# Optimization experiments

Hardware: AMD Instinct MI355X
Metric: run time of the kernel (lower is better)

The kernel has to match this reference:

```python
import jax, jax.numpy as jnp
import numpy as np
from jax import lax

B, S, F, D, H, L, A = 16, 512, 64, 512, 8, 4, 3
E = D // H  # head_dim = 64

def _gelu(t):
    return jax.nn.gelu(t, approximate=False)  # torch nn.GELU() is exact erf

def _make_masks():
    i = jnp.arange(S)[:, None]
    j = jnp.arange(S)[None, :]
    d = jnp.abs(i - j)
    ms = []
    for h in range(min(5, H)):
        dil = 2 ** h
        ms.append((d <= dil) | (d % (2 ** (h + 1)) == 0))
    m = jnp.stack(ms)  # [5,S,S] bool
    idx = jnp.minimum(jnp.arange(H), m.shape[0] - 1)
    return m[idx]  # [H,S,S]

MASKS = _make_masks()

def _ln(x, g, b, eps=1e-5):
    mu = jnp.mean(x, -1, keepdims=True)
    var = jnp.mean((x - mu) ** 2, -1, keepdims=True)
    return (x - mu) * lax.rsqrt(var + eps) * g + b

def _conv1d(x_ncw, w, b):
    y = lax.conv_general_dilated(x_ncw, w, (1,), [(1, 1)],
                                 dimension_numbers=("NCH", "OIH", "NCH"))
    return y + b[None, :, None]

def _attn(x, Wq, bq, Wk, bk, Wv, bv, Wo, bo):
    # x: [B,S,D]; Wq/Wk/Wv: [H,E,D] (stacked per-head Linear weights)
    q = jnp.einsum("bsd,hed->bhse", x, Wq) + bq[None, :, None, :]
    k = jnp.einsum("bsd,hed->bhse", x, Wk) + bk[None, :, None, :]
    v = jnp.einsum("bsd,hed->bhse", x, Wv) + bv[None, :, None, :]
    s = jnp.einsum("bhse,bhte->bhst", q, k) / (E ** 0.5)
    s = jnp.where(MASKS[None], s, -jnp.inf)  # log-sparse masked_fill
    p = jax.nn.softmax(s, axis=-1)
    o = jnp.einsum("bhst,bhte->bhse", p, v)
    o = o.transpose(0, 2, 1, 3).reshape(x.shape[0], x.shape[1], D)  # concat heads
    return o @ Wo.T + bo

def _forward(x, conv1_w, conv1_b, conv2_w, conv2_b, emb_w, emb_b, pos,
             Wq, bq, Wk, bk, Wv, bv, Wo, bo, ln1_g, ln1_b, ln2_g, ln2_b,
             W1, b1, W2, b2, lnf_g, lnf_b,
             a1_w, a1_b, a2_w, a2_b, a3_w, a3_b, a4_w, a4_b,
             c1_w, c1_b, c2_w, c2_b, c3_w, c3_b, c4_w, c4_b):
    # feature extractor: two conv1d+GELU over time axis
    h0 = _gelu(_conv1d(x.transpose(0, 2, 1), conv1_w, conv1_b))
    h0 = _gelu(_conv1d(h0, conv2_w, conv2_b)).transpose(0, 2, 1)  # [B,S,D]
    z = h0 @ emb_w.T + emb_b + pos[:, :S]  # input embedding + positional
    for l in range(L):  # PyraFormer blocks (pre-norm residual)
        z = z + _attn(_ln(z, ln1_g[l], ln1_b[l]),
                      Wq[l], bq[l], Wk[l], bk[l], Wv[l], bv[l], Wo[l], bo[l])
        h = _ln(z, ln2_g[l], ln2_b[l])
        z = z + (_gelu(h @ W1[l].T + b1[l]) @ W2[l].T + b2[l])
    z = _ln(z, lnf_g, lnf_b)
    feat = z[:, -1, :]  # last timestep features

    def head(f, layers):
        (w1, bb1), (w2, bb2), (w3, bb3), (w4, bb4) = layers
        f = _gelu(f @ w1.T + bb1)
        f = _gelu(f @ w2.T + bb2)
        f = _gelu(f @ w3.T + bb3)
        return f @ w4.T + bb4

    policy = head(feat, [(a1_w, a1_b), (a2_w, a2_b), (a3_w, a3_b), (a4_w, a4_b)])
    value = head(feat, [(c1_w, c1_b), (c2_w, c2_b), (c3_w, c3_b), (c4_w, c4_b)])
    return policy, value

def setup_inputs() -> dict:
    key = jax.random.key(0)
    ks = iter(jax.random.split(key, 64))
    r = lambda shape, s=0.05: jax.random.normal(next(ks), shape, jnp.float32) * s
    return {
        "x": jax.random.normal(next(ks), (B, S, F), jnp.float32),
        "conv1_w": r((D // 2, F, 3)), "conv1_b": jnp.zeros((D // 2,)),
        "conv2_w": r((D, D // 2, 3)), "conv2_b": jnp.zeros((D,)),
        "emb_w": r((D, D)), "emb_b": jnp.zeros((D,)),
        "pos": r((1, S, D), 0.02),
        "Wq": r((L, H, E, D)), "bq": jnp.zeros((L, H, E)),
        "Wk": r((L, H, E, D)), "bk": jnp.zeros((L, H, E)),
        "Wv": r((L, H, E, D)), "bv": jnp.zeros((L, H, E)),
        "Wo": r((L, D, D)), "bo": jnp.zeros((L, D)),
        "ln1_g": jnp.ones((L, D)), "ln1_b": jnp.zeros((L, D)),
        "ln2_g": jnp.ones((L, D)), "ln2_b": jnp.zeros((L, D)),
        "W1": r((L, 4 * D, D)), "b1": jnp.zeros((L, 4 * D)),
        "W2": r((L, D, 4 * D)), "b2": jnp.zeros((L, D)),
        "lnf_g": jnp.ones((D,)), "lnf_b": jnp.zeros((D,)),
        "a1_w": r((128, D)), "a1_b": jnp.zeros((128,)),
        "a2_w": r((256, 128)), "a2_b": jnp.zeros((256,)),
        "a3_w": r((57, 256)), "a3_b": jnp.zeros((57,)),
        "a4_w": r((A, 57)), "a4_b": jnp.zeros((A,)),
        "c1_w": r((128, D)), "c1_b": jnp.zeros((128,)),
        "c2_w": r((256, 128)), "c2_b": jnp.zeros((256,)),
        "c3_w": r((57, 256)), "c3_b": jnp.zeros((57,)),
        "c4_w": r((1, 57)), "c4_b": jnp.zeros((1,)),
    }

def reference(x, conv1_w, conv1_b, conv2_w, conv2_b, emb_w, emb_b, pos,
              Wq, bq, Wk, bk, Wv, bv, Wo, bo, ln1_g, ln1_b, ln2_g, ln2_b,
              W1, b1, W2, b2, lnf_g, lnf_b,
              a1_w, a1_b, a2_w, a2_b, a3_w, a3_b, a4_w, a4_b,
              c1_w, c1_b, c2_w, c2_b, c3_w, c3_b, c4_w, c4_b):
    return _forward(x, conv1_w, conv1_b, conv2_w, conv2_b, emb_w, emb_b, pos,
                    Wq, bq, Wk, bk, Wv, bv, Wo, bo, ln1_g, ln1_b, ln2_g, ln2_b,
                    W1, b1, W2, b2, lnf_g, lnf_b,
                    a1_w, a1_b, a2_w, a2_b, a3_w, a3_b, a4_w, a4_b,
                    c1_w, c1_b, c2_w, c2_b, c3_w, c3_b, c4_w, c4_b)
```

## Files before the change

kernel.cpp:

```cpp
#include <hip/hip_runtime.h>
#include <hip/hip_bf16.h>
#include <cstdint>

typedef __attribute__((ext_vector_type(8))) short bf16x8;
typedef __attribute__((ext_vector_type(4))) float f32x4;
typedef unsigned short u16;

#define DEV __device__ __forceinline__

DEV float b2f(u16 u) {
  union { unsigned int i; float f; } v; v.i = ((unsigned int)u) << 16; return v.f;
}
DEV u16 f2b(float f) {
  __hip_bfloat16 h = __float2bfloat16(f);
  return *reinterpret_cast<u16*>(&h);
}
DEV float erf_fast(float x) {
  float ax = fabsf(x);
  float t = __builtin_amdgcn_rcpf(fmaf(0.3275911f, ax, 1.0f));
  float p = t * fmaf(t, fmaf(t, fmaf(t, fmaf(t, 1.061405429f, -1.453152027f),
                                     1.421413741f), -0.284496736f), 0.254829592f);
  float r = fmaf(-p, __expf(-ax * ax), 1.0f);
  return copysignf(r, x);
}
DEV float gelu_f(float x) { return 0.5f * x * (1.0f + erf_fast(x * 0.70710678118654752f)); }

DEV void async_cp16(const u16* g, u16* l) {
  __builtin_amdgcn_global_load_lds(
      (const __attribute__((address_space(1))) void*)g,
      (__attribute__((address_space(3))) void*)l, 16, 0, 0);
}

__global__ void probe_kernel(const unsigned int* __restrict__ g, int* __restrict__ flag) {
  if (threadIdx.x == 0 && blockIdx.x == 0) *flag = (*g == 0x3F800000u) ? 1 : 0;
}

struct CvtArgs {
  const void* src[42];
  unsigned int off[43];
};

struct alignas(16) U8v { u16 u[8]; };
struct alignas(8)  U4v { u16 u[4]; };

__global__ __launch_bounds__(256) void cvt_kernel(CvtArgs a, int n_t, unsigned int total,
                                                  const int* __restrict__ flag,
                                                  u16* __restrict__ dst) {
  unsigned int i8 = (blockIdx.x * 256u + threadIdx.x) * 8u;
  if (i8 >= total) return;
  int t = 0;
  while (t + 1 < n_t && i8 >= a.off[t + 1]) t++;
  unsigned int j = i8 - a.off[t];
  bool in_seg = (i8 + 8 <= a.off[t + 1]) && (i8 + 8 <= total);
  int fp32 = *flag;
  if (fp32) {
    if (in_seg && ((j & 3) == 0)) {
      const float* s = (const float*)a.src[t] + j;
      float4 v0 = *(const float4*)s;
      float4 v1 = *(const float4*)(s + 4);
      U8v o;
      o.u[0] = f2b(v0.x); o.u[1] = f2b(v0.y); o.u[2] = f2b(v0.z); o.u[3] = f2b(v0.w);
      o.u[4] = f2b(v1.x); o.u[5] = f2b(v1.y); o.u[6] = f2b(v1.z); o.u[7] = f2b(v1.w);
      *(U8v*)(dst + i8) = o;
    } else {
      for (int k = 0; k < 8; k++) {
        unsigned int i = i8 + k;
        if (i >= total) break;
        int tt = t;
        while (tt + 1 < n_t && i >= a.off[tt + 1]) tt++;
        dst[i] = f2b(((const float*)a.src[tt])[i - a.off[tt]]);
      }
    }
  } else {
    if (in_seg && ((j & 7) == 0)) {
      *(U8v*)(dst + i8) = *(const U8v*)((const u16*)a.src[t] + j);
    } else {
      for (int k = 0; k < 8; k++) {
        unsigned int i = i8 + k;
        if (i >= total) break;
        int tt = t;
        while (tt + 1 < n_t && i >= a.off[tt + 1]) tt++;
        dst[i] = ((const u16*)a.src[tt])[i - a.off[tt]];
      }
    }
  }
}

__global__ __launch_bounds__(256) void gemm_bt44(
    const u16* __restrict__ A, const u16* __restrict__ W,
    const u16* __restrict__ bias,
    u16* __restrict__ outB, float* __restrict__ outF,
    int N, int K, int mode)
{
  __shared__ __align__(16) u16 As[2][64 * 32];
  __shared__ __align__(16) u16 Bs[2][64 * 32];
  int t = threadIdx.x, l = t & 63, w = t >> 6;
  int wr = w >> 1, wc = w & 1;
  int col = l & 15, quad = l >> 4;
  int q8 = (quad ^ ((col >> 1) & 3)) * 8;
  int m0 = blockIdx.x * 64;
  int n0 = blockIdx.y * 64;

  f32x4 acc[2][2];
#pragma unroll
  for (int i = 0; i < 2; i++)
#pragma unroll
    for (int j = 0; j < 2; j++) acc[i][j] = (f32x4){0.f, 0.f, 0.f, 0.f};

  int ra = t >> 2;
  int ca = (t & 3) ^ ((ra >> 1) & 3);
  const u16* a1 = A + (size_t)(m0 + ra) * K + ca * 8;
  const u16* b1 = W + (size_t)(n0 + ra) * K + ca * 8;

  int nK = K >> 5;
  async_cp16(a1, &As[0][t * 8]);
  async_cp16(b1, &Bs[0][t * 8]);
  for (int ki = 0; ki < nK; ki++) {
    int cur = ki & 1;
    if (ki + 1 < nK) {
      int nxt = cur ^ 1, kt = (ki + 1) << 5;
      async_cp16(a1 + kt, &As[nxt][t * 8]);
      async_cp16(b1 + kt, &Bs[nxt][t * 8]);
      __builtin_amdgcn_s_waitcnt(0x0F72);
    } else {
      __builtin_amdgcn_s_waitcnt(0x0F70);
    }
    __builtin_amdgcn_s_barrier();
    __builtin_amdgcn_sched_barrier(0);
    bf16x8 af[2], bfv[2];
#pragma unroll
    for (int mi = 0; mi < 2; mi++)
      af[mi] = *(const bf16x8*)&As[cur][(wr * 32 + mi * 16 + col) * 32 + q8];
#pragma unroll
    for (int ni = 0; ni < 2; ni++)
      bfv[ni] = *(const bf16x8*)&Bs[cur][(wc * 32 + ni * 16 + col) * 32 + q8];
#pragma unroll
    for (int mi = 0; mi < 2; mi++)
#pragma unroll
      for (int ni = 0; ni < 2; ni++)
        acc[mi][ni] = __builtin_amdgcn_mfma_f32_16x16x32_bf16(bfv[ni], af[mi], acc[mi][ni], 0, 0, 0);
    __builtin_amdgcn_sched_barrier(0);
    __builtin_amdgcn_s_barrier();
  }

  int mBase = m0 + wr * 32, nBase = n0 + wc * 32;
  if (mode == 1) {
#pragma unroll
    for (int mi = 0; mi < 2; mi++) {
      int m = mBase + mi * 16 + col;
      size_t rowOff = (size_t)m * N;
#pragma unroll
      for (int ni = 0; ni < 2; ni++) {
        int n4 = nBase + ni * 16 + quad * 4;
        U4v bb = *(const U4v*)&bias[n4];
        f32x4 v = acc[mi][ni];
        U4v o;
#pragma unroll
        for (int r = 0; r < 4; r++) o.u[r] = f2b(gelu_f(v[r] + b2f(bb.u[r])));
        *(U4v*)&outB[rowOff + n4] = o;
      }
    }
  } else {
#pragma unroll
    for (int mi = 0; mi < 2; mi++) {
      int m = mBase + mi * 16 + col;
      size_t rowOff = (size_t)m * N;
#pragma unroll
      for (int ni = 0; ni < 2; ni++) {
        int n4 = nBase + ni * 16 + quad * 4;
        U4v bb = *(const U4v*)&bias[n4];
        f32x4 v = acc[mi][ni];
        float4* p = (float4*)&outF[rowOff + n4];
        float4 zv = *p;
        zv.x += v[0] + b2f(bb.u[0]);
        zv.y += v[1] + b2f(bb.u[1]);
        zv.z += v[2] + b2f(bb.u[2]);
        zv.w += v[3] + b2f(bb.u[3]);
        *p = zv;
      }
    }
  }
}

__global__ __launch_bounds__(256) void gemm_qkv64(
    const u16* __restrict__ A,
    const u16* __restrict__ Wq, const u16* __restrict__ Wk, const u16* __restrict__ Wv,
    const u16* __restrict__ bq, const u16* __restrict__ bk, const u16* __restrict__ bv,
    u16* __restrict__ outQ, u16* __restrict__ outK, u16* __restrict__ outVT, int K)
{
  __shared__ __align__(16) u16 As[2][64 * 32];
  __shared__ __align__(16) u16 Bs[2][128 * 32];
  int t = threadIdx.x, l = t & 63, w = t >> 6;
  int wr = w >> 1, wc = w & 1;
  int col = l & 15, quad = l >> 4;
  int q8 = (quad ^ ((col >> 1) & 3)) * 8;
  int m0 = blockIdx.x * 64;
  int sel = blockIdx.y >> 2;
  int n0 = (blockIdx.y & 3) * 128;
  const u16* W = sel == 0 ? Wq : (sel == 1 ? Wk : Wv);
  const u16* bias = sel == 0 ? bq : (sel == 1 ? bk : bv);
  const bool swp = (sel < 2);
  const float scl = sel == 0 ? 0.125f : 1.0f;

  f32x4 acc[2][4];
#pragma unroll
  for (int i = 0; i < 2; i++)
#pragma unroll
    for (int j = 0; j < 4; j++) acc[i][j] = (f32x4){0.f, 0.f, 0.f, 0.f};

  int ra = t >> 2;
  int ca = (t & 3) ^ ((ra >> 1) & 3);
  int g1i = t, g2i = t + 256;
  int rb1 = g1i >> 2, rb2 = g2i >> 2;
  int cb1 = (g1i & 3) ^ ((rb1 >> 1) & 3);
  int cb2 = (g2i & 3) ^ ((rb2 >> 1) & 3);
  const u16* a1 = A + (size_t)(m0 + ra) * K + ca * 8;
  const u16* b1 = W + (size_t)(n0 + rb1) * K + cb1 * 8;
  const u16* b2 = W + (size_t)(n0 + rb2) * K + cb2 * 8;

  int nK = K >> 5;
  async_cp16(a1, &As[0][t * 8]);
  async_cp16(b1, &Bs[0][g1i * 8]);
  async_cp16(b2, &Bs[0][g2i * 8]);
  for (int ki = 0; ki < nK; ki++) {
    int cur = ki & 1;
    if (ki + 1 < nK) {
      int nxt = cur ^ 1, kt = (ki + 1) << 5;
      async_cp16(a1 + kt, &As[nxt][t * 8]);
      async_cp16(b1 + kt, &Bs[nxt][g1i * 8]);
      async_cp16(b2 + kt, &Bs[nxt][g2i * 8]);
      __builtin_amdgcn_s_waitcnt(0x0F73);
    } else {
      __builtin_amdgcn_s_waitcnt(0x0F70);
    }
    __builtin_amdgcn_s_barrier();
    __builtin_amdgcn_sched_barrier(0);
    bf16x8 af[2], bfv[4];
#pragma unroll
    for (int mi = 0; mi < 2; mi++)
      af[mi] = *(const bf16x8*)&As[cur][(wr * 32 + mi * 16 + col) * 32 + q8];
#pragma unroll
    for (int ni = 0; ni < 4; ni++)
      bfv[ni] = *(const bf16x8*)&Bs[cur][(wc * 64 + ni * 16 + col) * 32 + q8];
    if (swp) {
#pragma unroll
      for (int mi = 0; mi < 2; mi++)
#pragma unroll
        for (int ni = 0; ni < 4; ni++)
          acc[mi][ni] = __builtin_amdgcn_mfma_f32_16x16x32_bf16(bfv[ni], af[mi], acc[mi][ni], 0, 0, 0);
    } else {
#pragma unroll
      for (int mi = 0; mi < 2; mi++)
#pragma unroll
        for (int ni = 0; ni < 4; ni++)
          acc[mi][ni] = __builtin_amdgcn_mfma_f32_16x16x32_bf16(af[mi], bfv[ni], acc[mi][ni], 0, 0, 0);
    }
    __builtin_amdgcn_sched_barrier(0);
    __builtin_amdgcn_s_barrier();
  }

  int mBase = m0 + wr * 32, nBase = n0 + wc * 64;
  if (swp) {
    u16* outB = sel == 0 ? outQ : outK;
#pragma unroll
    for (int mi = 0; mi < 2; mi++) {
      int m = mBase + mi * 16 + col;
      size_t rowOff = (size_t)m * 512;
#pragma unroll
      for (int ni = 0; ni < 4; ni++) {
        int n4 = nBase + ni * 16 + quad * 4;
        U4v bb = *(const U4v*)&bias[n4];
        f32x4 v = acc[mi][ni];
        U4v o;
#pragma unroll
        for (int r = 0; r < 4; r++) o.u[r] = f2b((v[r] + b2f(bb.u[r])) * scl);
        *(U4v*)&outB[rowOff + n4] = o;
      }
    }
  } else {
    int b = m0 >> 9;
    int sB = m0 & 511;
#pragma unroll
    for (int mi = 0; mi < 2; mi++) {
      int s4 = sB + wr * 32 + mi * 16 + quad * 4;
#pragma unroll
      for (int ni = 0; ni < 4; ni++) {
        int n = nBase + ni * 16 + col;
        int h = n >> 6, e = n & 63;
        float bvv = b2f(bias[n]);
        f32x4 v = acc[mi][ni];
        U4v o;
#pragma unroll
        for (int r = 0; r < 4; r++) o.u[r] = f2b(v[r] + bvv);
        *(U4v*)&outVT[((size_t)((b * 8 + h) * 64 + e)) * 512 + s4] = o;
      }
    }
  }
}

__global__ __launch_bounds__(256) void zinit_kernel(const u16* __restrict__ pos,
                                                    float* __restrict__ z)
{
  int i = (blockIdx.x * 256 + threadIdx.x) * 8;
  int n = i & 511;
  int m = i >> 9;
  int s = m & 511;
  U8v p = *(const U8v*)&pos[s * 512 + n];
  float4 o0 = {b2f(p.u[0]), b2f(p.u[1]), b2f(p.u[2]), b2f(p.u[3])};
  float4 o1 = {b2f(p.u[4]), b2f(p.u[5]), b2f(p.u[6]), b2f(p.u[7])};
  *(float4*)(z + i) = o0;
  *(float4*)(z + i + 4) = o1;
}

__global__ void im2col3_kernel(const u16* __restrict__ src,
                               u16* __restrict__ dst, int C)
{
  int m = blockIdx.x;
  int k = blockIdx.y * blockDim.x + threadIdx.x;
  int ci = k / 3;
  int tap = k - ci * 3;
  int s = m & 511;
  int sp = s + tap - 1;
  u16 val = 0;
  if (sp >= 0 && sp < 512) val = src[(size_t)(m + tap - 1) * C + ci];
  dst[(size_t)m * (3 * C) + k] = val;
}

__global__ __launch_bounds__(256) void ln_kernel(
    const float* __restrict__ z, const u16* __restrict__ gam,
    const u16* __restrict__ bet, u16* __restrict__ out)
{
  int w = threadIdx.x >> 6, l = threadIdx.x & 63;
  int row = blockIdx.x * 4 + w;
  const float* zr = z + (size_t)row * 512;
  float4 v0 = *(const float4*)(zr + l * 8);
  float4 v1 = *(const float4*)(zr + l * 8 + 4);
  float x[8] = {v0.x, v0.y, v0.z, v0.w, v1.x, v1.y, v1.z, v1.w};
  float s = 0.f;
#pragma unroll
  for (int i = 0; i < 8; i++) s += x[i];
#pragma unroll
  for (int mm = 1; mm < 64; mm <<= 1) s += __shfl_xor(s, mm, 64);
  float mu = s * (1.0f / 512.0f);
  float vs = 0.f;
#pragma unroll
  for (int i = 0; i < 8; i++) { float d = x[i] - mu; vs += d * d; }
#pragma unroll
  for (int mm = 1; mm < 64; mm <<= 1) vs += __shfl_xor(vs, mm, 64);
  float rs = rsqrtf(vs * (1.0f / 512.0f) + 1e-5f);
  U8v gg = *(const U8v*)(gam + l * 8);
  U8v bb = *(const U8v*)(bet + l * 8);
  U8v o;
#pragma unroll
  for (int i = 0; i < 8; i++) o.u[i] = f2b((x[i] - mu) * rs * b2f(gg.u[i]) + b2f(bb.u[i]));
  *(U8v*)(out + (size_t)row * 512 + l * 8) = o;
}

__global__ __launch_bounds__(256) void lnf_kernel(
    const float* __restrict__ z, const u16* __restrict__ gam,
    const u16* __restrict__ bet, u16* __restrict__ feat)
{
  int w = threadIdx.x >> 6, l = threadIdx.x & 63;
  int b = blockIdx.x * 4 + w;
  const float* zr = z + ((size_t)b * 512 + 511) * 512;
  float4 v0 = *(const float4*)(zr + l * 8);
  float4 v1 = *(const float4*)(zr + l * 8 + 4);
  float x[8] = {v0.x, v0.y, v0.z, v0.w, v1.x, v1.y, v1.z, v1.w};
  float s = 0.f;
#pragma unroll
  for (int i = 0; i < 8; i++) s += x[i];
#pragma unroll
  for (int mm = 1; mm < 64; mm <<= 1) s += __shfl_xor(s, mm, 64);
  float mu = s * (1.0f / 512.0f);
  float vs = 0.f;
#pragma unroll
  for (int i = 0; i < 8; i++) { float d = x[i] - mu; vs += d * d; }
#pragma unroll
  for (int mm = 1; mm < 64; mm <<= 1) vs += __shfl_xor(vs, mm, 64);
  float rs = rsqrtf(vs * (1.0f / 512.0f) + 1e-5f);
  U8v gg = *(const U8v*)(gam + l * 8);
  U8v bb = *(const U8v*)(bet + l * 8);
  U8v o;
#pragma unroll
  for (int i = 0; i < 8; i++) o.u[i] = f2b((x[i] - mu) * rs * b2f(gg.u[i]) + b2f(bb.u[i]));
  *(U8v*)(feat + (size_t)b * 512 + l * 8) = o;
}

#define AST 72
__global__ __launch_bounds__(256) void attn_kernel(
    const u16* __restrict__ Q, const u16* __restrict__ Kg,
    const u16* __restrict__ VT, u16* __restrict__ O)
{
  __shared__ __align__(16) u16 Ks[64 * AST];
  __shared__ __align__(16) u16 Vts[64 * AST];
  __shared__ __align__(16) u16 Ps[64 * AST];
  const float NEG = -1e30f;
  int blk = blockIdx.x;
  int bh = blk & 127;
  int i0 = (blk >> 7) * 64;
  int b = bh >> 3, h = bh & 7;
  int t = threadIdx.x, w = t >> 6, l = t & 63;
  int col = l & 15, quad = l >> 4;
  int dil = 1 << (h < 4 ? h : 4);
  int per_m1 = 2 * dil - 1;

  {
    int row = t >> 2, c = (t & 3) * 16;
    const u16* src = Q + ((size_t)(b * 512 + i0 + row) * 512 + h * 64 + c);
    *(float4*)&Ps[row * AST + c] = *(const float4*)src;
    *(float4*)&Ps[row * AST + c + 8] = *(const float4*)(src + 8);
  }
  __builtin_amdgcn_s_waitcnt(0xC07F);
  __builtin_amdgcn_sched_barrier(0);
  bf16x8 qa[2];
#pragma unroll
  for (int kk = 0; kk < 2; kk++)
    qa[kk] = *(const bf16x8*)&Ps[(w * 16 + col) * AST + kk * 32 + quad * 8];

  f32x4 acc_o[4];
#pragma unroll
  for (int i = 0; i < 4; i++) acc_o[i] = (f32x4){0.f, 0.f, 0.f, 0.f};
  float m_run = NEG, l_run = 0.f;
  int ig = i0 + w * 16 + col;

  for (int jt = 0; jt < 8; jt++) {
    int j0 = jt * 64;
    {
      int row = t >> 2, c = (t & 3) * 16;
      const u16* ks = Kg + ((size_t)(b * 512 + j0 + row) * 512 + h * 64 + c);
      *(float4*)&Ks[row * AST + c] = *(const float4*)ks;
      *(float4*)&Ks[row * AST + c + 8] = *(const float4*)(ks + 8);
      const u16* vs = VT + ((size_t)(bh * 64 + row) * 512 + j0 + c);
      *(float4*)&Vts[row * AST + c] = *(const float4*)vs;
      *(float4*)&Vts[row * AST + c + 8] = *(const float4*)(vs + 8);
    }
    __syncthreads();

    f32x4 sa[4];
    __builtin_amdgcn_s_setprio(1);
#pragma unroll
    for (int ni = 0; ni < 4; ni++) {
      f32x4 s = (f32x4){0.f, 0.f, 0.f, 0.f};
#pragma unroll
      for (int kk = 0; kk < 2; kk++) {
        bf16x8 kb = *(const bf16x8*)&Ks[(ni * 16 + col) * AST + kk * 32 + quad * 8];
        s = __builtin_amdgcn_mfma_f32_16x16x32_bf16(kb, qa[kk], s, 0, 0, 0);
      }
      sa[ni] = s;
    }
    __builtin_amdgcn_s_setprio(0);

    float mx = NEG;
#pragma unroll
    for (int ni = 0; ni < 4; ni++)
#pragma unroll
      for (int r = 0; r < 4; r++) {
        int jg = j0 + ni * 16 + quad * 4 + r;
        int d = ig - jg; d = d < 0 ? -d : d;
        bool keep = (d <= dil) || ((d & per_m1) == 0);
        float s = keep ? sa[ni][r] : NEG;
        sa[ni][r] = s;
        mx = fmaxf(mx, s);
      }
    mx = fmaxf(mx, __shfl_xor(mx, 16, 64));
    mx = fmaxf(mx, __shfl_xor(mx, 32, 64));
    float mN = fmaxf(m_run, mx);
    float alpha = __expf(m_run - mN);
    m_run = mN;
    float rsum = 0.f;
#pragma unroll
    for (int ni = 0; ni < 4; ni++)
#pragma unroll
      for (int r = 0; r < 4; r++) {
        float p = __expf(sa[ni][r] - mN);
        sa[ni][r] = p;
        rsum += p;
      }
    rsum += __shfl_xor(rsum, 16, 64);
    rsum += __shfl_xor(rsum, 32, 64);
    l_run = l_run * alpha + rsum;

#pragma unroll
    for (int ni = 0; ni < 4; ni++) {
      unsigned int lo = (unsigned int)f2b(sa[ni][0]) | ((unsigned int)f2b(sa[ni][1]) << 16);
      unsigned int hi = (unsigned int)f2b(sa[ni][2]) | ((unsigned int)f2b(sa[ni][3]) << 16);
      uint2 pk; pk.x = lo; pk.y = hi;
      *(uint2*)&Ps[(w * 16 + col) * AST + ni * 16 + quad * 4] = pk;
    }
    __builtin_amdgcn_s_waitcnt(0xC07F);
    __builtin_amdgcn_sched_barrier(0);

    float a_sh[4];
#pragma unroll
    for (int r = 0; r < 4; r++) a_sh[r] = __shfl(alpha, quad * 4 + r, 64);
#pragma unroll
    for (int ne = 0; ne < 4; ne++)
#pragma unroll
      for (int r = 0; r < 4; r++) acc_o[ne][r] *= a_sh[r];

    bf16x8 pa[2];
#pragma unroll
    for (int kk = 0; kk < 2; kk++)
      pa[kk] = *(const bf16x8*)&Ps[(w * 16 + col) * AST + kk * 32 + quad * 8];
    __builtin_amdgcn_s_setprio(1);
#pragma unroll
    for (int ne = 0; ne < 4; ne++) {
#pragma unroll
      for (int kk = 0; kk < 2; kk++) {
        bf16x8 vb = *(const bf16x8*)&Vts[(ne * 16 + col) * AST + kk * 32 + quad * 8];
        acc_o[ne] = __builtin_amdgcn_mfma_f32_16x16x32_bf16(pa[kk], vb, acc_o[ne], 0, 0, 0);
      }
    }
    __builtin_amdgcn_s_setprio(0);
    __syncthreads();
  }

  float inv[4];
#pragma unroll
  for (int r = 0; r < 4; r++) {
    float lr = __shfl(l_run, quad * 4 + r, 64);
    inv[r] = 1.0f / fmaxf(lr, 1e-20f);
  }
#pragma unroll
  for (int ne = 0; ne < 4; ne++)
#pragma unroll
    for (int r = 0; r < 4; r++) {
      float o = acc_o[ne][r] * inv[r];
      O[((size_t)(b * 512 + i0 + w * 16 + quad * 4 + r)) * 512 + h * 64 + ne * 16 + col] = f2b(o);
    }
}

__global__ __launch_bounds__(256) void heads_kernel(
    const u16* __restrict__ feat,
    const u16* __restrict__ a1w, const u16* __restrict__ a1b,
    const u16* __restrict__ a2w, const u16* __restrict__ a2b,
    const u16* __restrict__ a3w, const u16* __restrict__ a3b,
    const u16* __restrict__ a4w, const u16* __restrict__ a4b,
    const u16* __restrict__ c1w, const u16* __restrict__ c1b,
    const u16* __restrict__ c2w, const u16* __restrict__ c2b,
    const u16* __restrict__ c3w, const u16* __restrict__ c3b,
    const u16* __restrict__ c4w, const u16* __restrict__ c4b,
    const int* __restrict__ flag, void* __restrict__ outv)
{
  __shared__ float f[512];
  __shared__ float g1[256];
  __shared__ float g2[512];
  __shared__ float g3[128];
  int b = blockIdx.x, t = threadIdx.x;
  f[t] = b2f(feat[b * 512 + t]);
  f[t + 256] = b2f(feat[b * 512 + 256 + t]);
  __syncthreads();
  {
    const u16* wrow; float bias;
    if (t < 128) { wrow = a1w + (size_t)t * 512; bias = b2f(a1b[t]); }
    else { wrow = c1w + (size_t)(t - 128) * 512; bias = b2f(c1b[t - 128]); }
    float s = bias;
    for (int k = 0; k < 512; k++) s += b2f(wrow[k]) * f[k];
    g1[t] = gelu_f(s);
  }
  __syncthreads();
  {
    float s1 = b2f(a2b[t]);
    for (int k = 0; k < 128; k++) s1 += b2f(a2w[t * 128 + k]) * g1[k];
    float s2 = b2f(c2b[t]);
    for (int k = 0; k < 128; k++) s2 += b2f(c2w[t * 128 + k]) * g1[128 + k];
    g2[t] = gelu_f(s1);
    g2[256 + t] = gelu_f(s2);
  }
  __syncthreads();
  if (t < 57) {
    float s = b2f(a3b[t]);
    for (int k = 0; k < 256; k++) s += b2f(a3w[t * 256 + k]) * g2[k];
    g3[t] = gelu_f(s);
  } else if (t >= 64 && t < 121) {
    int u = t - 64;
    float s = b2f(c3b[u]);
    for (int k = 0; k < 256; k++) s += b2f(c3w[u * 256 + k]) * g2[256 + k];
    g3[64 + u] = gelu_f(s);
  }
  __syncthreads();
  int fp32out = *flag;
  if (t < 3) {
    float s = b2f(a4b[t]);
    for (int k = 0; k < 57; k++) s += b2f(a4w[t * 57 + k]) * g3[k];
    if (fp32out) ((float*)outv)[b * 3 + t] = s;
    else ((u16*)outv)[b * 3 + t] = f2b(s);
  } else if (t == 4) {
    float s = b2f(c4b[0]);
    for (int k = 0; k < 57; k++) s += b2f(c4w[k]) * g3[64 + k];
    if (fp32out) ((float*)outv)[48 + b] = s;
    else ((u16*)outv)[48 + b] = f2b(s);
  }
}

extern "C" void kernel_launch(void* const* d_in, const int* in_sizes, int n_in,
                              void* d_out, int out_size, void* d_ws, size_t ws_size,
                              hipStream_t stream)
{
  char* ws = (char*)d_ws;
  float* z    = (float*)ws;
  u16* R      = (u16*)(ws + (16u << 20));
  u16* bufQ   = R;
  u16* bufK   = (u16*)(ws + (24u << 20));
  u16* bufO   = (u16*)(ws + (32u << 20));
  u16* bufVT  = (u16*)(ws + (40u << 20));
  u16* bufH   = (u16*)(ws + (48u << 20));
  u16* feat   = R;
  u16* pool   = (u16*)(ws + (56u << 20));
  int* flag   = (int*)(ws + (88u << 20));

  CvtArgs args;
  unsigned int off = 0;
  int nt = n_in < 42 ? n_in : 42;
  for (int i = 0; i < nt; i++) { args.src[i] = d_in[i]; args.off[i] = off; off += (unsigned int)in_sizes[i]; }
  args.off[nt] = off;
  unsigned int total = off;

  probe_kernel<<<1, 64, 0, stream>>>((const unsigned int*)d_in[24], flag);
  cvt_kernel<<<(total + 2047) / 2048, 256, 0, stream>>>(args, nt, total, flag, pool);

  const u16* P[42];
  for (int i = 0; i < nt; i++) P[i] = pool + args.off[i];
  const u16* x       = P[0];
  const u16* conv1_w = P[1];  const u16* conv1_b = P[2];
  const u16* conv2_w = P[3];  const u16* conv2_b = P[4];
  const u16* emb_w   = P[5];  const u16* emb_b   = P[6];
  const u16* pos     = P[7];
  const u16* Wq      = P[8];  const u16* bq      = P[9];
  const u16* Wk      = P[10]; const u16* bk      = P[11];
  const u16* Wv      = P[12]; const u16* bv      = P[13];
  const u16* Wo      = P[14]; const u16* bo      = P[15];
  const u16* ln1_g   = P[16]; const u16* ln1_b   = P[17];
  const u16* ln2_g   = P[18]; const u16* ln2_b   = P[19];
  const u16* W1      = P[20]; const u16* b1      = P[21];
  const u16* W2      = P[22]; const u16* b2      = P[23];
  const u16* lnf_g   = P[24]; const u16* lnf_b   = P[25];

  im2col3_kernel<<<dim3(8192, 1), 192, 0, stream>>>(x, R, 64);
  gemm_bt44<<<dim3(128, 4), 256, 0, stream>>>(R, conv1_w, conv1_b, bufH, nullptr, 256, 192, 1);
  im2col3_kernel<<<dim3(8192, 3), 256, 0, stream>>>(bufH, R, 256);
  gemm_bt44<<<dim3(128, 8), 256, 0, stream>>>(R, conv2_w, conv2_b, bufH, nullptr, 512, 768, 1);
  zinit_kernel<<<2048, 256, 0, stream>>>(pos, z);
  gemm_bt44<<<dim3(128, 8), 256, 0, stream>>>(bufH, emb_w, emb_b, nullptr, z, 512, 512, 2);

  for (int l = 0; l < 4; l++) {
    ln_kernel<<<2048, 256, 0, stream>>>(z, ln1_g + l * 512, ln1_b + l * 512, bufH);
    gemm_qkv64<<<dim3(128, 12), 256, 0, stream>>>(bufH,
        Wq + (size_t)l * 262144, Wk + (size_t)l * 262144, Wv + (size_t)l * 262144,
        bq + l * 512, bk + l * 512, bv + l * 512, bufQ, bufK, bufVT, 512);
    attn_kernel<<<dim3(1024), 256, 0, stream>>>(bufQ, bufK, bufVT, bufO);
    gemm_bt44<<<dim3(128, 8), 256, 0, stream>>>(bufO, Wo + (size_t)l * 262144, bo + l * 512, nullptr, z, 512, 512, 2);
    ln_kernel<<<2048, 256, 0, stream>>>(z, ln2_g + l * 512, ln2_b + l * 512, bufH);
    gemm_bt44<<<dim3(128, 32), 256, 0, stream>>>(bufH, W1 + (size_t)l * 1048576, b1 + l * 2048, R, nullptr, 2048, 512, 1);
    gemm_bt44<<<dim3(128, 8), 256, 0, stream>>>(R, W2 + (size_t)l * 1048576, b2 + l * 512, nullptr, z, 512, 2048, 2);
  }

  lnf_kernel<<<4, 256, 0, stream>>>(z, lnf_g, lnf_b, feat);
  heads_kernel<<<16, 256, 0, stream>>>(feat,
      P[26], P[27], P[28], P[29], P[30], P[31], P[32], P[33],
      P[34], P[35], P[36], P[37], P[38], P[39], P[40], P[41],
      flag, d_out);
}
```

Baseline: 902.2 us.

## Fuse pos-embedding into GEMM epilogue, enlarge QKV and FFN1 tiles, vectorize heads

The zinit kernel goes away: the embedding GEMM gains a new epilogue mode that adds the positional table and writes z directly instead of read-modify-writing it. The QKV projection now uses 64x256 tiles instead of 64x128, and the first FFN GEMM gets a new 128x64 tile kernel. Both changes aim to raise operand reuse per block and cut the block count. The heads kernel now reads weights as 8-wide vectors. The larger tiles raise register and LDS use, which could lower occupancy, and fewer blocks may underfill the CUs.

```diff
diff --git a/kernel.cpp b/kernel.cpp
--- a/kernel.cpp
+++ b/kernel.cpp
@@ -90,6 +90,7 @@
     const u16* __restrict__ A, const u16* __restrict__ W,
     const u16* __restrict__ bias,
     u16* __restrict__ outB, float* __restrict__ outF,
+    const u16* __restrict__ pos,
     int N, int K, int mode)
 {
   __shared__ __align__(16) u16 As[2][64 * 32];
@@ -160,7 +161,7 @@
         *(U4v*)&outB[rowOff + n4] = o;
       }
     }
-  } else {
+  } else if (mode == 2) {
 #pragma unroll
     for (int mi = 0; mi < 2; mi++) {
       int m = mBase + mi * 16 + col;
@@ -179,87 +180,192 @@
         *p = zv;
       }
     }
-  }
-}
-
-__global__ __launch_bounds__(256) void gemm_qkv64(
+  } else {
+#pragma unroll
+    for (int mi = 0; mi < 2; mi++) {
+      int m = mBase + mi * 16 + col;
+      int s = m & 511;
+      size_t rowOff = (size_t)m * N;
+#pragma unroll
+      for (int ni = 0; ni < 2; ni++) {
+        int n4 = nBase + ni * 16 + quad * 4;
+        U4v bb = *(const U4v*)&bias[n4];
+        U4v pp = *(const U4v*)&pos[s * 512 + n4];
+        f32x4 v = acc[mi][ni];
+        float4 zv;
+        zv.x = v[0] + b2f(bb.u[0]) + b2f(pp.u[0]);
+        zv.y = v[1] + b2f(bb.u[1]) + b2f(pp.u[1]);
+        zv.z = v[2] + b2f(bb.u[2]) + b2f(pp.u[2]);
+        zv.w = v[3] + b2f(bb.u[3]) + b2f(pp.u[3]);
+        *(float4*)&outF[rowOff + n4] = zv;
+      }
+    }
+  }
+}
+
+__global__ __launch_bounds__(256) void gemm_bt128x64(
+    const u16* __restrict__ A, const u16* __restrict__ W,
+    const u16* __restrict__ bias,
+    u16* __restrict__ outB, int N, int K)
+{
+  __shared__ __align__(16) u16 As[2][128 * 32];
+  __shared__ __align__(16) u16 Bs[2][64 * 32];
+  int t = threadIdx.x, l = t & 63, w = t >> 6;
+  int wr = w >> 1, wc = w & 1;
+  int col = l & 15, quad = l >> 4;
+  int q8 = (quad ^ ((col >> 1) & 3)) * 8;
+  int m0 = blockIdx.x * 128;
+  int n0 = blockIdx.y * 64;
+
+  f32x4 acc[4][2];
+#pragma unroll
+  for (int i = 0; i < 4; i++)
+#pragma unroll
+    for (int j = 0; j < 2; j++) acc[i][j] = (f32x4){0.f, 0.f, 0.f, 0.f};
+
+  int g1i = t, g2i = t + 256;
+  int r1 = g1i >> 2, r2 = g2i >> 2;
+  int cb1 = (g1i & 3) ^ ((r1 >> 1) & 3);
+  int cb2 = (g2i & 3) ^ ((r2 >> 1) & 3);
+  int rb = t >> 2;
+  int cbb = (t & 3) ^ ((rb >> 1) & 3);
+  const u16* a1 = A + (size_t)(m0 + r1) * K + cb1 * 8;
+  const u16* a2 = A + (size_t)(m0 + r2) * K + cb2 * 8;
+  const u16* b1 = W + (size_t)(n0 + rb) * K + cbb * 8;
+
+  int nK = K >> 5;
+  async_cp16(a1, &As[0][g1i * 8]);
+  async_cp16(a2, &As[0][g2i * 8]);
+  async_cp16(b1, &Bs[0][t * 8]);
+  for (int ki = 0; ki < nK; ki++) {
+    int cur = ki & 1;
+    if (ki + 1 < nK) {
+      int nxt = cur ^ 1, kt = (ki + 1) << 5;
+      async_cp16(a1 + kt, &As[nxt][g1i * 8]);
+      async_cp16(a2 + kt, &As[nxt][g2i * 8]);
+      async_cp16(b1 + kt, &Bs[nxt][t * 8]);
+      __builtin_amdgcn_s_waitcnt(0x0F73);
+    } else {
+      __builtin_amdgcn_s_waitcnt(0x0F70);
+    }
+    __builtin_amdgcn_s_barrier();
+    __builtin_amdgcn_sched_barrier(0);
+    bf16x8 af[4], bfv[2];
+#pragma unroll
+    for (int mi = 0; mi < 4; mi++)
+      af[mi] = *(const bf16x8*)&As[cur][(wr * 64 + mi * 16 + col) * 32 + q8];
+#pragma unroll
+    for (int ni = 0; ni < 2; ni++)
+      bfv[ni] = *(const bf16x8*)&Bs[cur][(wc * 32 + ni * 16 + col) * 32 + q8];
+#pragma unroll
+    for (int mi = 0; mi < 4; mi++)
+#pragma unroll
+      for (int ni = 0; ni < 2; ni++)
+        acc[mi][ni] = __builtin_amdgcn_mfma_f32_16x16x32_bf16(bfv[ni], af[mi], acc[mi][ni], 0, 0, 0);
+    __builtin_amdgcn_sched_barrier(0);
+    __builtin_amdgcn_s_barrier();
+  }
+
+  int mBase = m0 + wr * 64, nBase = n0 + wc * 32;
+#pragma unroll
+  for (int mi = 0; mi < 4; mi++) {
+    int m = mBase + mi * 16 + col;
+    size_t rowOff = (size_t)m * N;
+#pragma unroll
+    for (int ni = 0; ni < 2; ni++) {
+      int n4 = nBase + ni * 16 + quad * 4;
+      U4v bb = *(const U4v*)&bias[n4];
+      f32x4 v = acc[mi][ni];
+      U4v o;
+#pragma unroll
+      for (int r = 0; r < 4; r++) o.u[r] = f2b(gelu_f(v[r] + b2f(bb.u[r])));
+      *(U4v*)&outB[rowOff + n4] = o;
+    }
+  }
+}
+
+__global__ __launch_bounds__(256) void gemm_qkv256(
     const u16* __restrict__ A,
     const u16* __restrict__ Wq, const u16* __restrict__ Wk, const u16* __restrict__ Wv,
     const u16* __restrict__ bq, const u16* __restrict__ bk, const u16* __restrict__ bv,
     u16* __restrict__ outQ, u16* __restrict__ outK, u16* __restrict__ outVT, int K)
 {
   __shared__ __align__(16) u16 As[2][64 * 32];
-  __shared__ __align__(16) u16 Bs[2][128 * 32];
+  __shared__ __align__(16) u16 Bs[2][256 * 32];
   int t = threadIdx.x, l = t & 63, w = t >> 6;
   int wr = w >> 1, wc = w & 1;
   int col = l & 15, quad = l >> 4;
   int q8 = (quad ^ ((col >> 1) & 3)) * 8;
   int m0 = blockIdx.x * 64;
-  int sel = blockIdx.y >> 2;
-  int n0 = (blockIdx.y & 3) * 128;
+  int sel = blockIdx.y >> 1;
+  int n0 = (blockIdx.y & 1) * 256;
   const u16* W = sel == 0 ? Wq : (sel == 1 ? Wk : Wv);
   const u16* bias = sel == 0 ? bq : (sel == 1 ? bk : bv);
   const bool swp = (sel < 2);
   const float scl = sel == 0 ? 0.125f : 1.0f;
 
-  f32x4 acc[2][4];
+  f32x4 acc[2][8];
 #pragma unroll
   for (int i = 0; i < 2; i++)
 #pragma unroll
-    for (int j = 0; j < 4; j++) acc[i][j] = (f32x4){0.f, 0.f, 0.f, 0.f};
+    for (int j = 0; j < 8; j++) acc[i][j] = (f32x4){0.f, 0.f, 0.f, 0.f};
 
   int ra = t >> 2;
   int ca = (t & 3) ^ ((ra >> 1) & 3);
-  int g1i = t, g2i = t + 256;
-  int rb1 = g1i >> 2, rb2 = g2i >> 2;
-  int cb1 = (g1i & 3) ^ ((rb1 >> 1) & 3);
-  int cb2 = (g2i & 3) ^ ((rb2 >> 1) & 3);
   const u16* a1 = A + (size_t)(m0 + ra) * K + ca * 8;
-  const u16* b1 = W + (size_t)(n0 + rb1) * K + cb1 * 8;
-  const u16* b2 = W + (size_t)(n0 + rb2) * K + cb2 * 8;
+  const u16* bptr[4];
+  int bidx[4];
+#pragma unroll
+  for (int j = 0; j < 4; j++) {
+    int gi = t + 256 * j;
+    int rb = gi >> 2;
+    int cb = (gi & 3) ^ ((rb >> 1) & 3);
+    bptr[j] = W + (size_t)(n0 + rb) * K + cb * 8;
+    bidx[j] = gi;
+  }
 
   int nK = K >> 5;
   async_cp16(a1, &As[0][t * 8]);
-  async_cp16(b1, &Bs[0][g1i * 8]);
-  async_cp16(b2, &Bs[0][g2i * 8]);
+#pragma unroll
+  for (int j = 0; j < 4; j++) async_cp16(bptr[j], &Bs[0][bidx[j] * 8]);
   for (int ki = 0; ki < nK; ki++) {
     int cur = ki & 1;
     if (ki + 1 < nK) {
       int nxt = cur ^ 1, kt = (ki + 1) << 5;
       async_cp16(a1 + kt, &As[nxt][t * 8]);
-      async_cp16(b1 + kt, &Bs[nxt][g1i * 8]);
-      async_cp16(b2 + kt, &Bs[nxt][g2i * 8]);
-      __builtin_amdgcn_s_waitcnt(0x0F73);
+#pragma unroll
+      for (int j = 0; j < 4; j++) async_cp16(bptr[j] + kt, &Bs[nxt][bidx[j] * 8]);
+      __builtin_amdgcn_s_waitcnt(0x0F75);
     } else {
       __builtin_amdgcn_s_waitcnt(0x0F70);
     }
     __builtin_amdgcn_s_barrier();
     __builtin_amdgcn_sched_barrier(0);
-    bf16x8 af[2], bfv[4];
+    bf16x8 af[2], bfv[8];
 #pragma unroll
     for (int mi = 0; mi < 2; mi++)
       af[mi] = *(const bf16x8*)&As[cur][(wr * 32 + mi * 16 + col) * 32 + q8];
 #pragma unroll
-    for (int ni = 0; ni < 4; ni++)
-      bfv[ni] = *(const bf16x8*)&Bs[cur][(wc * 64 + ni * 16 + col) * 32 + q8];
+    for (int ni = 0; ni < 8; ni++)
+      bfv[ni] = *(const bf16x8*)&Bs[cur][(wc * 128 + ni * 16 + col) * 32 + q8];
     if (swp) {
 #pragma unroll
       for (int mi = 0; mi < 2; mi++)
 #pragma unroll
-        for (int ni = 0; ni < 4; ni++)
+        for (int ni = 0; ni < 8; ni++)
           acc[mi][ni] = __builtin_amdgcn_mfma_f32_16x16x32_bf16(bfv[ni], af[mi], acc[mi][ni], 0, 0, 0);
     } else {
 #pragma unroll
       for (int mi = 0; mi < 2; mi++)
 #pragma unroll
-        for (int ni = 0; ni < 4; ni++)
+        for (int ni = 0; ni < 8; ni++)
           acc[mi][ni] = __builtin_amdgcn_mfma_f32_16x16x32_bf16(af[mi], bfv[ni], acc[mi][ni], 0, 0, 0);
     }
     __builtin_amdgcn_sched_barrier(0);
     __builtin_amdgcn_s_barrier();
   }
 
-  int mBase = m0 + wr * 32, nBase = n0 + wc * 64;
+  int mBase = m0 + wr * 32, nBase = n0 + wc * 128;
   if (swp) {
     u16* outB = sel == 0 ? outQ : outK;
 #pragma unroll
@@ -267,7 +373,7 @@
       int m = mBase + mi * 16 + col;
       size_t rowOff = (size_t)m * 512;
 #pragma unroll
-      for (int ni = 0; ni < 4; ni++) {
+      for (int ni = 0; ni < 8; ni++) {
         int n4 = nBase + ni * 16 + quad * 4;
         U4v bb = *(const U4v*)&bias[n4];
         f32x4 v = acc[mi][ni];
@@ -284,7 +390,7 @@
     for (int mi = 0; mi < 2; mi++) {
       int s4 = sB + wr * 32 + mi * 16 + quad * 4;
 #pragma unroll
-      for (int ni = 0; ni < 4; ni++) {
+      for (int ni = 0; ni < 8; ni++) {
         int n = nBase + ni * 16 + col;
         int h = n >> 6, e = n & 63;
         float bvv = b2f(bias[n]);
@@ -296,20 +402,6 @@
       }
     }
   }
-}
-
-__global__ __launch_bounds__(256) void zinit_kernel(const u16* __restrict__ pos,
-                                                    float* __restrict__ z)
-{
-  int i = (blockIdx.x * 256 + threadIdx.x) * 8;
-  int n = i & 511;
-  int m = i >> 9;
-  int s = m & 511;
-  U8v p = *(const U8v*)&pos[s * 512 + n];
-  float4 o0 = {b2f(p.u[0]), b2f(p.u[1]), b2f(p.u[2]), b2f(p.u[3])};
-  float4 o1 = {b2f(p.u[4]), b2f(p.u[5]), b2f(p.u[6]), b2f(p.u[7])};
-  *(float4*)(z + i) = o0;
-  *(float4*)(z + i + 4) = o1;
 }
 
 __global__ void im2col3_kernel(const u16* __restrict__ src,
@@ -555,27 +647,47 @@
     if (t < 128) { wrow = a1w + (size_t)t * 512; bias = b2f(a1b[t]); }
     else { wrow = c1w + (size_t)(t - 128) * 512; bias = b2f(c1b[t - 128]); }
     float s = bias;
-    for (int k = 0; k < 512; k++) s += b2f(wrow[k]) * f[k];
+    for (int k = 0; k < 512; k += 8) {
+      U8v wv = *(const U8v*)(wrow + k);
+#pragma unroll
+      for (int j = 0; j < 8; j++) s += b2f(wv.u[j]) * f[k + j];
+    }
     g1[t] = gelu_f(s);
   }
   __syncthreads();
   {
     float s1 = b2f(a2b[t]);
-    for (int k = 0; k < 128; k++) s1 += b2f(a2w[t * 128 + k]) * g1[k];
+    for (int k = 0; k < 128; k += 8) {
+      U8v wv = *(const U8v*)(a2w + (size_t)t * 128 + k);
+#pragma unroll
+      for (int j = 0; j < 8; j++) s1 += b2f(wv.u[j]) * g1[k + j];
+    }
     float s2 = b2f(c2b[t]);
-    for (int k = 0; k < 128; k++) s2 += b2f(c2w[t * 128 + k]) * g1[128 + k];
+    for (int k = 0; k < 128; k += 8) {
+      U8v wv = *(const U8v*)(c2w + (size_t)t * 128 + k);
+#pragma unroll
+      for (int j = 0; j < 8; j++) s2 += b2f(wv.u[j]) * g1[128 + k + j];
+    }
     g2[t] = gelu_f(s1);
     g2[256 + t] = gelu_f(s2);
   }
   __syncthreads();
   if (t < 57) {
     float s = b2f(a3b[t]);
-    for (int k = 0; k < 256; k++) s += b2f(a3w[t * 256 + k]) * g2[k];
+    for (int k = 0; k < 256; k += 8) {
+      U8v wv = *(const U8v*)(a3w + (size_t)t * 256 + k);
+#pragma unroll
+      for (int j = 0; j < 8; j++) s += b2f(wv.u[j]) * g2[k + j];
+    }
     g3[t] = gelu_f(s);
   } else if (t >= 64 && t < 121) {
     int u = t - 64;
     float s = b2f(c3b[u]);
-    for (int k = 0; k < 256; k++) s += b2f(c3w[u * 256 + k]) * g2[256 + k];
+    for (int k = 0; k < 256; k += 8) {
+      U8v wv = *(const U8v*)(c3w + (size_t)u * 256 + k);
+#pragma unroll
+      for (int j = 0; j < 8; j++) s += b2f(wv.u[j]) * g2[256 + k + j];
+    }
     g3[64 + u] = gelu_f(s);
   }
   __syncthreads();
@@ -637,22 +749,21 @@
   const u16* lnf_g   = P[24]; const u16* lnf_b   = P[25];
 
   im2col3_kernel<<<dim3(8192, 1), 192, 0, stream>>>(x, R, 64);
-  gemm_bt44<<<dim3(128, 4), 256, 0, stream>>>(R, conv1_w, conv1_b, bufH, nullptr, 256, 192, 1);
+  gemm_bt44<<<dim3(128, 4), 256, 0, stream>>>(R, conv1_w, conv1_b, bufH, nullptr, nullptr, 256, 192, 1);
   im2col3_kernel<<<dim3(8192, 3), 256, 0, stream>>>(bufH, R, 256);
-  gemm_bt44<<<dim3(128, 8), 256, 0, stream>>>(R, conv2_w, conv2_b, bufH, nullptr, 512, 768, 1);
-  zinit_kernel<<<2048, 256, 0, stream>>>(pos, z);
-  gemm_bt44<<<dim3(128, 8), 256, 0, stream>>>(bufH, emb_w, emb_b, nullptr, z, 512, 512, 2);
+  gemm_bt44<<<dim3(128, 8), 256, 0, stream>>>(R, conv2_w, conv2_b, bufH, nullptr, nullptr, 512, 768, 1);
+  gemm_bt44<<<dim3(128, 8), 256, 0, stream>>>(bufH, emb_w, emb_b, nullptr, z, pos, 512, 512, 4);
 
   for (int l = 0; l < 4; l++) {
     ln_kernel<<<2048, 256, 0, stream>>>(z, ln1_g + l * 512, ln1_b + l * 512, bufH);
-    gemm_qkv64<<<dim3(128, 12), 256, 0, stream>>>(bufH,
+    gemm_qkv256<<<dim3(128, 6), 256, 0, stream>>>(bufH,
         Wq + (size_t)l * 262144, Wk + (size_t)l * 262144, Wv + (size_t)l * 262144,
         bq + l * 512, bk + l * 512, bv + l * 512, bufQ, bufK, bufVT, 512);
     attn_kernel<<<dim3(1024), 256, 0, stream>>>(bufQ, bufK, bufVT, bufO);
-    gemm_bt44<<<dim3(128, 8), 256, 0, stream>>>(bufO, Wo + (size_t)l * 262144, bo + l * 512, nullptr, z, 512, 512, 2);
+    gemm_bt44<<<dim3(128, 8), 256, 0, stream>>>(bufO, Wo + (size_t)l * 262144, bo + l * 512, nullptr, z, nullptr, 512, 512, 2);
     ln_kernel<<<2048, 256, 0, stream>>>(z, ln2_g + l * 512, ln2_b + l * 512, bufH);
-    gemm_bt44<<<dim3(128, 32), 256, 0, stream>>>(bufH, W1 + (size_t)l * 1048576, b1 + l * 2048, R, nullptr, 2048, 512, 1);
-    gemm_bt44<<<dim3(128, 8), 256, 0, stream>>>(R, W2 + (size_t)l * 1048576, b2 + l * 512, nullptr, z, 512, 2048, 2);
+    gemm_bt128x64<<<dim3(64, 32), 256, 0, stream>>>(bufH, W1 + (size_t)l * 1048576, b1 + l * 2048, R, 2048, 512);
+    gemm_bt44<<<dim3(128, 8), 256, 0, stream>>>(R, W2 + (size_t)l * 1048576, b2 + l * 512, nullptr, z, nullptr, 512, 2048, 2);
   }
 
   lnf_kernel<<<4, 256, 0, stream>>>(z, lnf_g, lnf_b, feat);
```

Result: no change. 913.6 us (+1.3%).
